# Optimization experiments

Hardware: AMD Instinct MI355X
Metric: run time of the kernel (lower is better)

The kernel has to match this reference:

```python
import jax, jax.numpy as jnp
import numpy as np

B = 64        # graphs in batch
N = 2048      # nodes per graph (uniform -> static pooled sizes)
DEG = 16      # avg degree
E = B * N * DEG
F0 = 128      # node feature dim


def setup_inputs() -> dict:
    key = jax.random.key(0)
    ks = jax.random.split(key, 24)
    x = jax.random.normal(ks[0], (B * N, F0), dtype=jnp.float32)
    # within-graph random edges, PyG batched-graph layout (contiguous node blocks)
    loc = jax.random.randint(ks[1], (2, B, N * DEG), 0, N)
    off = (jnp.arange(B, dtype=jnp.int32) * N)[:, None]
    src = (loc[0].astype(jnp.int32) + off).reshape(-1)
    dst = (loc[1].astype(jnp.int32) + off).reshape(-1)
    g = lambda i, shp: jax.random.normal(ks[i], shp, dtype=jnp.float32) * 0.05
    return {
        'x': x, 'src': src, 'dst': dst,
        'w1l': g(2, (128, 128)), 'b1': jnp.zeros((128,), jnp.float32), 'w1r': g(3, (128, 128)), 'pw1': g(4, (128,)),
        'w2l': g(5, (128, 128)), 'b2': jnp.zeros((128,), jnp.float32), 'w2r': g(6, (128, 128)), 'pw2': g(7, (128,)),
        'w3l': g(8, (128, 128)), 'b3': jnp.zeros((128,), jnp.float32), 'w3r': g(9, (128, 128)), 'pw3': g(10, (128,)),
        'l1w': g(11, (256, 128)), 'l1b': jnp.zeros((128,), jnp.float32),
        'l2w': g(12, (128, 64)), 'l2b': jnp.zeros((64,), jnp.float32),
        'l3w': g(13, (64, 2)), 'l3b': jnp.zeros((2,), jnp.float32),
    }


def _sage(x, src, dst, em, n_nodes, Wl, b, Wr):
    # PyG SAGEConv: lin_l(mean_{j->i} x_j) + lin_r(x_i); edge mask zeroes dropped edges
    msg = x[src] * em[:, None]                                   # [E, F] gather
    agg = jax.ops.segment_sum(msg, dst, num_segments=n_nodes)
    cnt = jax.ops.segment_sum(em, dst, num_segments=n_nodes)
    mean = agg / jnp.maximum(cnt, 1.0)[:, None]
    return mean @ Wl + b + x @ Wr


def _topk_pool(x, src, dst, em, b_graphs, n_per, w):
    # PyG TopKPooling (min_score=None): score = tanh(x@w/||w||), keep top ratio per graph,
    # gate kept features by score, drop edges touching removed nodes, relabel.
    score = jnp.tanh((x @ w) / jnp.linalg.norm(w))
    k = n_per // 2                                               # ratio = 0.5
    _, idx = jax.lax.top_k(score.reshape(b_graphs, n_per), k)    # per-graph local idx
    perm = (jnp.arange(b_graphs, dtype=jnp.int32)[:, None] * n_per + idx.astype(jnp.int32)).reshape(-1)
    xn = x[perm] * score[perm][:, None]
    ntot = b_graphs * n_per
    kept = jnp.zeros((ntot,), bool).at[perm].set(True)
    newidx = jnp.zeros((ntot,), jnp.int32).at[perm].set(jnp.arange(b_graphs * k, dtype=jnp.int32))
    emn = em * kept[src].astype(em.dtype) * kept[dst].astype(em.dtype)
    return xn, newidx[src], newidx[dst], emn, k


def _readout(x, b_graphs, n_per):
    r = x.reshape(b_graphs, n_per, -1)
    return jnp.concatenate([r.max(axis=1), r.mean(axis=1)], axis=1)  # [B, 2F]


def _forward(x, src, dst, w1l, b1, w1r, pw1, w2l, b2, w2r, pw2, w3l, b3, w3r, pw3,
             l1w, l1b, l2w, l2b, l3w, l3b):
    em = jnp.ones((src.shape[0],), x.dtype)
    n = N
    h = jax.nn.relu(_sage(x, src, dst, em, B * n, w1l, b1, w1r))
    h, src, dst, em, n = _topk_pool(h, src, dst, em, B, n, pw1)
    x1 = _readout(h, B, n)
    h = jax.nn.relu(_sage(h, src, dst, em, B * n, w2l, b2, w2r))
    h, src, dst, em, n = _topk_pool(h, src, dst, em, B, n, pw2)
    x2 = _readout(h, B, n)
    h = jax.nn.relu(_sage(h, src, dst, em, B * n, w3l, b3, w3r))
    h, src, dst, em, n = _topk_pool(h, src, dst, em, B, n, pw3)
    x3 = _readout(h, B, n)
    z = x1 + x2 + x3
    z = jax.nn.relu(z @ l1w + l1b)            # dropout is identity in eval mode
    z = jax.nn.relu(z @ l2w + l2b)
    z = z @ l3w + l3b
    return jax.nn.log_softmax(z, axis=-1)


def reference(x, src, dst, w1l, b1, w1r, pw1, w2l, b2, w2r, pw2, w3l, b3, w3r, pw3,
              l1w, l1b, l2w, l2b, l3w, l3b):
    return _forward(x, src, dst, w1l, b1, w1r, pw1, w2l, b2, w2r, pw2, w3l, b3, w3r, pw3,
                    l1w, l1b, l2w, l2b, l3w, l3b)
```

## Files before the change

kernel.cpp:

```cpp
#include <hip/hip_runtime.h>
#include <cmath>

#define NT1  131072
#define ETOT 2097152
#define NB   64
#define F    128
#define CPAD 32
#define RCH  16

__global__ void hist_kernel(const int* __restrict__ dst, int* __restrict__ deg) {
  int e = blockIdx.x * blockDim.x + threadIdx.x;
  if (e < ETOT) atomicAdd(&deg[dst[e]], 1);
}

__global__ void scan1_kernel(const int* __restrict__ deg, int* __restrict__ rowstart,
                             int* __restrict__ bsum) {
  __shared__ int ls[256];
  int base = blockIdx.x * 1024;
  int t = threadIdx.x;
  int i = base + t * 4;
  int a0 = deg[i], a1 = deg[i + 1], a2 = deg[i + 2], a3 = deg[i + 3];
  int s = a0 + a1 + a2 + a3;
  ls[t] = s;
  __syncthreads();
  for (int off = 1; off < 256; off <<= 1) {
    int v = (t >= off) ? ls[t - off] : 0;
    __syncthreads();
    ls[t] += v;
    __syncthreads();
  }
  int excl = ls[t] - s;
  rowstart[i]     = excl;
  rowstart[i + 1] = excl + a0;
  rowstart[i + 2] = excl + a0 + a1;
  rowstart[i + 3] = excl + a0 + a1 + a2;
  if (t == 255) bsum[blockIdx.x] = ls[255];
}

__global__ void scan2_kernel(int* __restrict__ bsum) {
  __shared__ int ls[128];
  int t = threadIdx.x;
  int v0 = bsum[t];
  ls[t] = v0;
  __syncthreads();
  for (int off = 1; off < 128; off <<= 1) {
    int v = (t >= off) ? ls[t - off] : 0;
    __syncthreads();
    ls[t] += v;
    __syncthreads();
  }
  bsum[t] = ls[t] - v0;
}

__global__ void scan3_kernel(int* __restrict__ rowstart, const int* __restrict__ bsum) {
  int base = blockIdx.x * 1024;
  int off = bsum[blockIdx.x];
  int i = base + threadIdx.x * 4;
  rowstart[i] += off; rowstart[i + 1] += off; rowstart[i + 2] += off; rowstart[i + 3] += off;
}

__global__ void fill_kernel(const int* __restrict__ src, const int* __restrict__ dst,
                            const int* __restrict__ rowstart, int* __restrict__ cursor,
                            int* __restrict__ csr) {
  int e = blockIdx.x * blockDim.x + threadIdx.x;
  if (e < ETOT) {
    int d = dst[e];
    int pos = rowstart[d] + atomicAdd(&cursor[d], 1);
    csr[pos] = src[e];
  }
}

__global__ void init_id_kernel(int* __restrict__ m, int* __restrict__ orig,
                               const int* __restrict__ rowstart,
                               const int* __restrict__ deg, int2* __restrict__ sd2) {
  int v = blockIdx.x * blockDim.x + threadIdx.x;
  m[v] = v; orig[v] = v;
  sd2[v] = make_int2(rowstart[v], deg[v]);
}

__global__ void map_kernel(const int* __restrict__ csr, const int* __restrict__ m,
                           int* __restrict__ mcsr) {
  int e = blockIdx.x * blockDim.x + threadIdx.x;
  int4 v = ((const int4*)csr)[e];
  int4 o;
  o.x = m[v.x]; o.y = m[v.y]; o.z = m[v.z]; o.w = m[v.w];
  ((int4*)mcsr)[e] = o;
}

__global__ __launch_bounds__(256) void agg_kernel(
    const float* __restrict__ xin, const int* __restrict__ mcsr,
    const int2* __restrict__ sd2, float* __restrict__ agg,
    const float* __restrict__ pw, float* __restrict__ invn) {
  if (blockIdx.x == 0 && threadIdx.x < 64) {
    int l = threadIdx.x;
    float vv = pw[l] * pw[l] + pw[l + 64] * pw[l + 64];
    #pragma unroll
    for (int o = 32; o; o >>= 1) vv += __shfl_xor(vv, o);
    if (l == 0) *invn = 1.0f / sqrtf(vv);
  }
  int swz = gridDim.x >> 3;
  int nb  = (blockIdx.x & 7) * swz + (blockIdx.x >> 3);
  int g = threadIdx.x >> 5, l = threadIdx.x & 31;
  int jd = nb * 8 + g;
  int2 sdv = sd2[jd];
  int s = sdv.x, d = sdv.y;
  float4 acc = make_float4(0.f, 0.f, 0.f, 0.f);
  int c = 0;
  for (int base = 0; base < d; base += 32) {
    int dc = min(32, d - base);
    int nbid = (l < dc) ? mcsr[s + base + l] : -1;
    int j = 0;
    for (; j + 4 <= dc; j += 4) {
      int n0 = __shfl(nbid, j, 32);
      int n1 = __shfl(nbid, j + 1, 32);
      int n2 = __shfl(nbid, j + 2, 32);
      int n3 = __shfl(nbid, j + 3, 32);
      float4 v0 = *(const float4*)(xin + (size_t)max(n0, 0) * F + l * 4);
      float4 v1 = *(const float4*)(xin + (size_t)max(n1, 0) * F + l * 4);
      float4 v2 = *(const float4*)(xin + (size_t)max(n2, 0) * F + l * 4);
      float4 v3 = *(const float4*)(xin + (size_t)max(n3, 0) * F + l * 4);
      if (n0 >= 0) { acc.x += v0.x; acc.y += v0.y; acc.z += v0.z; acc.w += v0.w; ++c; }
      if (n1 >= 0) { acc.x += v1.x; acc.y += v1.y; acc.z += v1.z; acc.w += v1.w; ++c; }
      if (n2 >= 0) { acc.x += v2.x; acc.y += v2.y; acc.z += v2.z; acc.w += v2.w; ++c; }
      if (n3 >= 0) { acc.x += v3.x; acc.y += v3.y; acc.z += v3.z; acc.w += v3.w; ++c; }
    }
    for (; j < dc; ++j) {
      int n0 = __shfl(nbid, j, 32);
      if (n0 >= 0) {
        float4 v0 = *(const float4*)(xin + (size_t)n0 * F + l * 4);
        acc.x += v0.x; acc.y += v0.y; acc.z += v0.z; acc.w += v0.w; ++c;
      }
    }
  }
  float inv = 1.0f / (float)max(c, 1);
  acc.x *= inv; acc.y *= inv; acc.z *= inv; acc.w *= inv;
  *(float4*)(agg + (size_t)jd * F + l * 4) = acc;
}

__global__ __launch_bounds__(256) void sage_gemm(
    const float* agg, const float* __restrict__ x,
    const float* __restrict__ Wl, const float* __restrict__ Wr,
    const float* __restrict__ bias, float* h,
    const float* __restrict__ pw, const float* __restrict__ invn,
    float* __restrict__ score) {
  __shared__ float At[16][132];
  __shared__ float Wt[16][132];
  int t  = threadIdx.x;
  int tx = t & 15, ty = t >> 4;
  int i0 = blockIdx.x * 128;
  int arow = t & 127, akc = (t >> 7) * 8;
  int wkr  = t >> 4,  wc0 = (t & 15) * 8;

  float acc[8][8];
  #pragma unroll
  for (int r = 0; r < 8; ++r)
    #pragma unroll
    for (int c = 0; c < 8; ++c) acc[r][c] = 0.f;

  for (int kt = 0; kt < 256; kt += 16) {
    const float* Asrc = (kt < 128) ? agg : x;
    int acol = (kt & 127) + akc;
    float4 va0 = *(const float4*)(Asrc + (size_t)(i0 + arow) * F + acol);
    float4 va1 = *(const float4*)(Asrc + (size_t)(i0 + arow) * F + acol + 4);
    const float* Wsrc = ((kt < 128) ? Wl : Wr) + (size_t)((kt & 127) + wkr) * F + wc0;
    float4 vw0 = *(const float4*)(Wsrc);
    float4 vw1 = *(const float4*)(Wsrc + 4);
    __syncthreads();
    At[akc + 0][arow] = va0.x; At[akc + 1][arow] = va0.y;
    At[akc + 2][arow] = va0.z; At[akc + 3][arow] = va0.w;
    At[akc + 4][arow] = va1.x; At[akc + 5][arow] = va1.y;
    At[akc + 6][arow] = va1.z; At[akc + 7][arow] = va1.w;
    Wt[wkr][wc0 + 0] = vw0.x; Wt[wkr][wc0 + 1] = vw0.y;
    Wt[wkr][wc0 + 2] = vw0.z; Wt[wkr][wc0 + 3] = vw0.w;
    Wt[wkr][wc0 + 4] = vw1.x; Wt[wkr][wc0 + 5] = vw1.y;
    Wt[wkr][wc0 + 6] = vw1.z; Wt[wkr][wc0 + 7] = vw1.w;
    __syncthreads();
    #pragma unroll
    for (int k = 0; k < 16; ++k) {
      float4 a0 = *(float4*)(&At[k][ty * 4]);
      float4 a1 = *(float4*)(&At[k][64 + ty * 4]);
      float4 w0 = *(float4*)(&Wt[k][tx * 4]);
      float4 w1 = *(float4*)(&Wt[k][64 + tx * 4]);
      float ar[8] = {a0.x, a0.y, a0.z, a0.w, a1.x, a1.y, a1.z, a1.w};
      float wr[8] = {w0.x, w0.y, w0.z, w0.w, w1.x, w1.y, w1.z, w1.w};
      #pragma unroll
      for (int r = 0; r < 8; ++r)
        #pragma unroll
        for (int c = 0; c < 8; ++c)
          acc[r][c] += ar[r] * wr[c];
    }
  }

  float4 bb0 = *(const float4*)(bias + tx * 4);
  float4 bb1 = *(const float4*)(bias + 64 + tx * 4);
  float4 pw0 = *(const float4*)(pw + tx * 4);
  float4 pw1 = *(const float4*)(pw + 64 + tx * 4);
  float inorm = *invn;
  #pragma unroll
  for (int r = 0; r < 8; ++r) {
    int row = i0 + ((r < 4) ? (ty * 4 + r) : (64 + ty * 4 + r - 4));
    float4 o0, o1;
    o0.x = fmaxf(acc[r][0] + bb0.x, 0.f);
    o0.y = fmaxf(acc[r][1] + bb0.y, 0.f);
    o0.z = fmaxf(acc[r][2] + bb0.z, 0.f);
    o0.w = fmaxf(acc[r][3] + bb0.w, 0.f);
    o1.x = fmaxf(acc[r][4] + bb1.x, 0.f);
    o1.y = fmaxf(acc[r][5] + bb1.y, 0.f);
    o1.z = fmaxf(acc[r][6] + bb1.z, 0.f);
    o1.w = fmaxf(acc[r][7] + bb1.w, 0.f);
    *(float4*)(h + (size_t)row * F + tx * 4) = o0;
    *(float4*)(h + (size_t)row * F + 64 + tx * 4) = o1;
    float p = o0.x * pw0.x + o0.y * pw0.y + o0.z * pw0.z + o0.w * pw0.w
            + o1.x * pw1.x + o1.y * pw1.y + o1.z * pw1.z + o1.w * pw1.w;
    #pragma unroll
    for (int off = 8; off; off >>= 1) p += __shfl_xor(p, off);
    if (tx == 0) score[row] = tanhf(p * inorm);
  }
}

__global__ void topk_kernel(const float* __restrict__ score, float* __restrict__ thr,
                            int* __restrict__ quota, int* __restrict__ tiecur,
                            int* __restrict__ curg, int nper, int k) {
  __shared__ float s[2048];
  __shared__ int cnts[256];
  int b = blockIdx.x, tid = threadIdx.x;
  for (int i = tid; i < nper; i += 256) s[i] = score[b * nper + i];
  __syncthreads();
  for (int size = 2; size <= nper; size <<= 1)
    for (int stride = size >> 1; stride; stride >>= 1) {
      for (int i = tid; i < nper; i += 256) {
        int j = i ^ stride;
        if (j > i) {
          bool up = ((i & size) == 0);
          float a = s[i], c = s[j];
          if ((a > c) == up) { s[i] = c; s[j] = a; }
        }
      }
      __syncthreads();
    }
  float T = s[nper - k];
  int c = 0;
  for (int i = tid; i < nper; i += 256) c += (s[i] > T) ? 1 : 0;
  cnts[tid] = c;
  __syncthreads();
  for (int st = 128; st; st >>= 1) {
    if (tid < st) cnts[tid] += cnts[tid + st];
    __syncthreads();
  }
  if (tid == 0) { thr[b] = T; quota[b] = k - cnts[0]; tiecur[b * CPAD] = 0; curg[b * CPAD] = 0; }
}

__global__ __launch_bounds__(256) void select_kernel(
    const float* __restrict__ h, const float* __restrict__ score,
    const float* __restrict__ thr, const int* __restrict__ quota,
    int* __restrict__ tiecur, int* __restrict__ curg,
    const int* __restrict__ origA, int* __restrict__ origB,
    int* __restrict__ m, float* __restrict__ xnext,
    const int* __restrict__ rowstart, const int* __restrict__ deg,
    int2* __restrict__ sd2, int nper, int k) {
  __shared__ int   snid[64];
  __shared__ float ssc[64];
  int t = threadIdx.x;
  int base = blockIdx.x * 64;
  int b = base / nper;
  if (t < 64) {
    int i = base + t;
    float sc = score[i];
    float T = thr[b];
    int keep = (sc > T) ? 1 : 0;
    if (!keep && sc == T) keep = (atomicAdd(&tiecur[b * CPAD], 1) < quota[b]) ? 1 : 0;
    unsigned long long mask = __ballot(keep);
    int pre = __popcll(mask & ((1ull << t) - 1ull));
    int tot = __popcll(mask);
    int wbase = 0;
    if (t == 0 && tot) wbase = atomicAdd(&curg[b * CPAD], tot);
    wbase = __shfl(wbase, 0);
    int nid = keep ? (b * k + wbase + pre) : -1;
    int orig = origA[i];
    m[orig] = nid;
    if (nid >= 0) {
      origB[nid] = orig;
      sd2[nid] = make_int2(rowstart[orig], deg[orig]);
    }
    snid[t] = nid; ssc[t] = sc;
  }
  __syncthreads();
  int g = t >> 5, l32 = t & 31;
  for (int n = g; n < 64; n += 8) {
    int nid = snid[n];
    if (nid >= 0) {
      float sc = ssc[n];
      float4 v = *(const float4*)(h + (size_t)(base + n) * F + l32 * 4);
      v.x *= sc; v.y *= sc; v.z *= sc; v.w *= sc;
      *(float4*)(xnext + (size_t)nid * F + l32 * 4) = v;
    }
  }
}

__global__ __launch_bounds__(256) void readout_partial(
    const float* __restrict__ xp, float* __restrict__ pmax,
    float* __restrict__ psum, int k) {
  __shared__ float smax[256], ssum[256];
  int b  = blockIdx.x >> 4;
  int ch = blockIdx.x & 15;
  int t  = threadIdx.x;
  int rg = t >> 7, f = t & 127;
  int rows = k >> 4;
  int r0 = ch * rows;
  const float* base = xp + ((size_t)b * k + r0) * F;
  float mx = -INFINITY, sm = 0.f;
  #pragma unroll 4
  for (int r = rg; r < rows; r += 2) {
    float v = base[(size_t)r * F + f];
    mx = fmaxf(mx, v);
    sm += v;
  }
  smax[t] = mx; ssum[t] = sm;
  __syncthreads();
  if (t < 128) {
    int o = (b * 16 + ch) * 128 + t;
    pmax[o] = fmaxf(smax[t], smax[t + 128]);
    psum[o] = ssum[t] + ssum[t + 128];
  }
}

__global__ void readout_final(const float* __restrict__ pmax,
                              const float* __restrict__ psum,
                              float* __restrict__ z, int k) {
  int b = blockIdx.x, f = threadIdx.x;
  float mx = -INFINITY, sm = 0.f;
  #pragma unroll
  for (int ch = 0; ch < 16; ++ch) {
    int o = (b * 16 + ch) * 128 + f;
    mx = fmaxf(mx, pmax[o]);
    sm += psum[o];
  }
  z[b * 256 + f]       += mx;
  z[b * 256 + 128 + f] += sm / (float)k;
}

__global__ void mlp_kernel(const float* __restrict__ z,
                           const float* __restrict__ l1w, const float* __restrict__ l1b,
                           const float* __restrict__ l2w, const float* __restrict__ l2b,
                           const float* __restrict__ l3w, const float* __restrict__ l3b,
                           float* __restrict__ out) {
  int b = blockIdx.x, t = threadIdx.x;
  __shared__ float zz[256], o1[128], o2[64], lg[2];
  zz[t]       = z[b * 256 + t];
  zz[t + 128] = z[b * 256 + 128 + t];
  __syncthreads();
  float a = l1b[t];
  for (int i = 0; i < 256; ++i) a += zz[i] * l1w[i * 128 + t];
  o1[t] = fmaxf(a, 0.f);
  __syncthreads();
  if (t < 64) {
    float a2 = l2b[t];
    for (int i = 0; i < 128; ++i) a2 += o1[i] * l2w[i * 64 + t];
    o2[t] = fmaxf(a2, 0.f);
  }
  __syncthreads();
  if (t < 2) {
    float a3 = l3b[t];
    for (int i = 0; i < 64; ++i) a3 += o2[i] * l3w[i * 2 + t];
    lg[t] = a3;
  }
  __syncthreads();
  if (t == 0) {
    float mmax = fmaxf(lg[0], lg[1]);
    float lse = mmax + logf(expf(lg[0] - mmax) + expf(lg[1] - mmax));
    out[b * 2 + 0] = lg[0] - lse;
    out[b * 2 + 1] = lg[1] - lse;
  }
}

extern "C" void kernel_launch(void* const* d_in, const int* in_sizes, int n_in,
                              void* d_out, int out_size, void* d_ws, size_t ws_size,
                              hipStream_t stream) {
  const float* x   = (const float*)d_in[0];
  const int*   src = (const int*)d_in[1];
  const int*   dst = (const int*)d_in[2];
  const float* Wl[3] = {(const float*)d_in[3], (const float*)d_in[7],  (const float*)d_in[11]};
  const float* bs[3] = {(const float*)d_in[4], (const float*)d_in[8],  (const float*)d_in[12]};
  const float* Wr[3] = {(const float*)d_in[5], (const float*)d_in[9],  (const float*)d_in[13]};
  const float* pw[3] = {(const float*)d_in[6], (const float*)d_in[10], (const float*)d_in[14]};
  const float* l1w = (const float*)d_in[15]; const float* l1b = (const float*)d_in[16];
  const float* l2w = (const float*)d_in[17]; const float* l2b = (const float*)d_in[18];
  const float* l3w = (const float*)d_in[19]; const float* l3b = (const float*)d_in[20];
  float* out = (float*)d_out;

  char* p = (char*)d_ws;
  auto take = [&](size_t bytes) { char* q = p; p += (bytes + 255) & ~(size_t)255; return q; };
  float* aggh   = (float*)take((size_t)NT1 * F * 4);
  float* xbuf   = (float*)take((size_t)65536 * F * 4);
  float* score  = (float*)take((size_t)NT1 * 4);
  int* deg      = (int*)take((size_t)NT1 * 4);
  int* rowstart = (int*)take((size_t)NT1 * 4);
  int* cursor   = (int*)take((size_t)NT1 * 4);
  int* m        = (int*)take((size_t)NT1 * 4);
  int* origA    = (int*)take((size_t)NT1 * 4);
  int* origB    = (int*)take((size_t)NT1 * 4);
  int2* sd2     = (int2*)take((size_t)NT1 * 8);
  int* csr      = (int*)take((size_t)ETOT * 4);
  int* mcsr     = (int*)take((size_t)ETOT * 4);
  int* bsum     = (int*)take(128 * 4);
  float* thr    = (float*)take(NB * 4);
  int* quota    = (int*)take(NB * 4);
  int* tiecur   = (int*)take(NB * CPAD * 4);
  int* curg     = (int*)take(NB * CPAD * 4);
  float* z      = (float*)take(NB * 256 * 4);
  float* pmax   = (float*)take((size_t)NB * RCH * F * 4);
  float* psum   = (float*)take((size_t)NB * RCH * F * 4);
  float* invn   = (float*)take(4);

  hipMemsetAsync(deg, 0, (size_t)NT1 * 4, stream);
  hipMemsetAsync(cursor, 0, (size_t)NT1 * 4, stream);
  hipMemsetAsync(z, 0, (size_t)NB * 256 * 4, stream);

  hist_kernel<<<ETOT / 256, 256, 0, stream>>>(dst, deg);
  scan1_kernel<<<128, 256, 0, stream>>>(deg, rowstart, bsum);
  scan2_kernel<<<1, 128, 0, stream>>>(bsum);
  scan3_kernel<<<128, 256, 0, stream>>>(rowstart, bsum);
  fill_kernel<<<ETOT / 256, 256, 0, stream>>>(src, dst, rowstart, cursor, csr);
  init_id_kernel<<<NT1 / 256, 256, 0, stream>>>(m, origA, rowstart, deg, sd2);

  int NT = NT1, nper = 2048;
  const float* xin = x;
  int* oin = origA; int* oout = origB;
  for (int s = 0; s < 3; ++s) {
    int k = nper / 2;
    const int* edges = csr;
    if (s > 0) {
      map_kernel<<<ETOT / 4 / 256, 256, 0, stream>>>(csr, m, mcsr);
      edges = mcsr;
    }
    agg_kernel<<<NT / 8, 256, 0, stream>>>(xin, edges, sd2, aggh, pw[s], invn);
    sage_gemm<<<NT / 128, 256, 0, stream>>>(aggh, xin, Wl[s], Wr[s], bs[s], aggh,
                                            pw[s], invn, score);
    topk_kernel<<<NB, 256, 0, stream>>>(score, thr, quota, tiecur, curg, nper, k);
    select_kernel<<<NT / 64, 256, 0, stream>>>(aggh, score, thr, quota, tiecur, curg,
                                               oin, oout, m, xbuf, rowstart, deg, sd2,
                                               nper, k);
    readout_partial<<<NB * RCH, 256, 0, stream>>>(xbuf, pmax, psum, k);
    readout_final<<<NB, 128, 0, stream>>>(pmax, psum, z, k);
    NT = NB * k; nper = k; xin = xbuf;
    int* tmp = oin; oin = oout; oout = tmp;
  }
  mlp_kernel<<<NB, 128, 0, stream>>>(z, l1w, l1b, l2w, l2b, l3w, l3b, out);
}
```

Measured before the change: 763.1 us.

## Use radix-select top-k, double-buffer SAGE GEMM, fuse readout into select

The per-graph bitonic sort in topk is replaced with an 8-bit radix select over order-preserving uint keys, which finds the k-th score threshold and tie quota with far fewer shared-memory passes. sage_gemm is templated on row-tile size, uses double-buffered shared tiles with register prefetch of the next K tile, and uses 64-row tiles for the smaller pooled stages so more blocks are launched. The readout partial max and sum are folded into select_kernel, which removes the readout_partial launch and a re-read of the pooled features. The cost is a more complex GEMM with extra shared memory and per-block partials sized by MAXBLK.

```diff
diff --git a/kernel.cpp b/kernel.cpp
--- a/kernel.cpp
+++ b/kernel.cpp
@@ -6,7 +6,7 @@
 #define NB   64
 #define F    128
 #define CPAD 32
-#define RCH  16
+#define MAXBLK 32
 
 __global__ void hist_kernel(const int* __restrict__ dst, int* __restrict__ deg) {
   int e = blockIdx.x * blockDim.x + threadIdx.x;
@@ -137,57 +137,76 @@
   *(float4*)(agg + (size_t)jd * F + l * 4) = acc;
 }
 
+template <int BM>
 __global__ __launch_bounds__(256) void sage_gemm(
     const float* agg, const float* __restrict__ x,
     const float* __restrict__ Wl, const float* __restrict__ Wr,
     const float* __restrict__ bias, float* h,
     const float* __restrict__ pw, const float* __restrict__ invn,
     float* __restrict__ score) {
-  __shared__ float At[16][132];
-  __shared__ float Wt[16][132];
+  constexpr int RQ = BM / 64;
+  __shared__ float At[2][16][BM + 4];
+  __shared__ float Wt[2][16][132];
   int t  = threadIdx.x;
   int tx = t & 15, ty = t >> 4;
-  int i0 = blockIdx.x * 128;
-  int arow = t & 127, akc = (t >> 7) * 8;
-  int wkr  = t >> 4,  wc0 = (t & 15) * 8;
-
-  float acc[8][8];
+  int i0 = blockIdx.x * BM;
+  int arow, akc;
+  if (BM == 128) { arow = t & 127; akc = (t >> 7) * 8; }
+  else           { arow = t & 63;  akc = (t >> 6) * 4; }
+  int wkr = t >> 4, wc0 = (t & 15) * 8;
+
+  float4 va0, va1, vw0, vw1;
+  auto loadT = [&](int ktile) {
+    const float* Asrc = (ktile < 8) ? agg : x;
+    int acol = (ktile & 7) * 16 + akc;
+    const float* pA = Asrc + (size_t)(i0 + arow) * F + acol;
+    va0 = *(const float4*)pA;
+    if (BM == 128) va1 = *(const float4*)(pA + 4);
+    const float* Wsrc = ((ktile < 8) ? Wl : Wr) + (size_t)((ktile & 7) * 16 + wkr) * F + wc0;
+    vw0 = *(const float4*)Wsrc;
+    vw1 = *(const float4*)(Wsrc + 4);
+  };
+
+  float acc[4 * RQ][8];
   #pragma unroll
-  for (int r = 0; r < 8; ++r)
+  for (int r = 0; r < 4 * RQ; ++r)
     #pragma unroll
     for (int c = 0; c < 8; ++c) acc[r][c] = 0.f;
 
-  for (int kt = 0; kt < 256; kt += 16) {
-    const float* Asrc = (kt < 128) ? agg : x;
-    int acol = (kt & 127) + akc;
-    float4 va0 = *(const float4*)(Asrc + (size_t)(i0 + arow) * F + acol);
-    float4 va1 = *(const float4*)(Asrc + (size_t)(i0 + arow) * F + acol + 4);
-    const float* Wsrc = ((kt < 128) ? Wl : Wr) + (size_t)((kt & 127) + wkr) * F + wc0;
-    float4 vw0 = *(const float4*)(Wsrc);
-    float4 vw1 = *(const float4*)(Wsrc + 4);
-    __syncthreads();
-    At[akc + 0][arow] = va0.x; At[akc + 1][arow] = va0.y;
-    At[akc + 2][arow] = va0.z; At[akc + 3][arow] = va0.w;
-    At[akc + 4][arow] = va1.x; At[akc + 5][arow] = va1.y;
-    At[akc + 6][arow] = va1.z; At[akc + 7][arow] = va1.w;
-    Wt[wkr][wc0 + 0] = vw0.x; Wt[wkr][wc0 + 1] = vw0.y;
-    Wt[wkr][wc0 + 2] = vw0.z; Wt[wkr][wc0 + 3] = vw0.w;
-    Wt[wkr][wc0 + 4] = vw1.x; Wt[wkr][wc0 + 5] = vw1.y;
-    Wt[wkr][wc0 + 6] = vw1.z; Wt[wkr][wc0 + 7] = vw1.w;
-    __syncthreads();
+  loadT(0);
+  for (int kt = 0; kt < 16; ++kt) {
+    int buf = kt & 1;
+    At[buf][akc + 0][arow] = va0.x; At[buf][akc + 1][arow] = va0.y;
+    At[buf][akc + 2][arow] = va0.z; At[buf][akc + 3][arow] = va0.w;
+    if (BM == 128) {
+      At[buf][akc + 4][arow] = va1.x; At[buf][akc + 5][arow] = va1.y;
+      At[buf][akc + 6][arow] = va1.z; At[buf][akc + 7][arow] = va1.w;
+    }
+    *(float4*)(&Wt[buf][wkr][wc0]) = vw0;
+    *(float4*)(&Wt[buf][wkr][wc0 + 4]) = vw1;
+    __syncthreads();
+    if (kt < 15) loadT(kt + 1);
     #pragma unroll
     for (int k = 0; k < 16; ++k) {
-      float4 a0 = *(float4*)(&At[k][ty * 4]);
-      float4 a1 = *(float4*)(&At[k][64 + ty * 4]);
-      float4 w0 = *(float4*)(&Wt[k][tx * 4]);
-      float4 w1 = *(float4*)(&Wt[k][64 + tx * 4]);
-      float ar[8] = {a0.x, a0.y, a0.z, a0.w, a1.x, a1.y, a1.z, a1.w};
+      float4 a0 = *(float4*)(&At[buf][k][ty * 4]);
+      float4 w0 = *(float4*)(&Wt[buf][k][tx * 4]);
+      float4 w1 = *(float4*)(&Wt[buf][k][64 + tx * 4]);
       float wr[8] = {w0.x, w0.y, w0.z, w0.w, w1.x, w1.y, w1.z, w1.w};
+      float ar0[4] = {a0.x, a0.y, a0.z, a0.w};
       #pragma unroll
-      for (int r = 0; r < 8; ++r)
+      for (int r = 0; r < 4; ++r)
         #pragma unroll
         for (int c = 0; c < 8; ++c)
-          acc[r][c] += ar[r] * wr[c];
+          acc[r][c] += ar0[r] * wr[c];
+      if (RQ == 2) {
+        float4 a1 = *(float4*)(&At[buf][k][64 + ty * 4]);
+        float ar1[4] = {a1.x, a1.y, a1.z, a1.w};
+        #pragma unroll
+        for (int r = 0; r < 4; ++r)
+          #pragma unroll
+          for (int c = 0; c < 8; ++c)
+            acc[4 + r][c] += ar1[r] * wr[c];
+      }
     }
   }
 
@@ -197,7 +216,7 @@
   float4 pw1 = *(const float4*)(pw + 64 + tx * 4);
   float inorm = *invn;
   #pragma unroll
-  for (int r = 0; r < 8; ++r) {
+  for (int r = 0; r < 4 * RQ; ++r) {
     int row = i0 + ((r < 4) ? (ty * 4 + r) : (64 + ty * 4 + r - 4));
     float4 o0, o1;
     o0.x = fmaxf(acc[r][0] + bb0.x, 0.f);
@@ -218,36 +237,51 @@
   }
 }
 
-__global__ void topk_kernel(const float* __restrict__ score, float* __restrict__ thr,
-                            int* __restrict__ quota, int* __restrict__ tiecur,
-                            int* __restrict__ curg, int nper, int k) {
-  __shared__ float s[2048];
-  __shared__ int cnts[256];
-  int b = blockIdx.x, tid = threadIdx.x;
-  for (int i = tid; i < nper; i += 256) s[i] = score[b * nper + i];
-  __syncthreads();
-  for (int size = 2; size <= nper; size <<= 1)
-    for (int stride = size >> 1; stride; stride >>= 1) {
-      for (int i = tid; i < nper; i += 256) {
-        int j = i ^ stride;
-        if (j > i) {
-          bool up = ((i & size) == 0);
-          float a = s[i], c = s[j];
-          if ((a > c) == up) { s[i] = c; s[j] = a; }
-        }
-      }
+__global__ __launch_bounds__(256) void topk_kernel(
+    const float* __restrict__ score, float* __restrict__ thr,
+    int* __restrict__ quota, int* __restrict__ tiecur,
+    int* __restrict__ curg, int nper, int k) {
+  __shared__ unsigned su[2048];
+  __shared__ int hist[256];
+  __shared__ int vsel;
+  int b = blockIdx.x, t = threadIdx.x;
+  for (int i = t; i < nper; i += 256) {
+    unsigned u = __float_as_uint(score[b * nper + i]);
+    su[i] = (u & 0x80000000u) ? ~u : (u | 0x80000000u);
+  }
+  __syncthreads();
+  unsigned prefix = 0;
+  int rem = k;
+  for (int shift = 24; shift >= 0; shift -= 8) {
+    hist[t] = 0;
+    __syncthreads();
+    unsigned maskhi = (shift == 24) ? 0u : (0xFFFFFFFFu << (shift + 8));
+    for (int i = t; i < nper; i += 256) {
+      unsigned u = su[i];
+      if ((u & maskhi) == prefix) atomicAdd(&hist[(u >> shift) & 255], 1);
+    }
+    __syncthreads();
+    for (int off = 1; off < 256; off <<= 1) {
+      int v = (t + off < 256) ? hist[t + off] : 0;
       __syncthreads();
-    }
-  float T = s[nper - k];
-  int c = 0;
-  for (int i = tid; i < nper; i += 256) c += (s[i] > T) ? 1 : 0;
-  cnts[tid] = c;
-  __syncthreads();
-  for (int st = 128; st; st >>= 1) {
-    if (tid < st) cnts[tid] += cnts[tid + st];
-    __syncthreads();
-  }
-  if (tid == 0) { thr[b] = T; quota[b] = k - cnts[0]; tiecur[b * CPAD] = 0; curg[b * CPAD] = 0; }
+      hist[t] += v;
+      __syncthreads();
+    }
+    if (hist[t] >= rem && (t == 255 || hist[t + 1] < rem)) vsel = t;
+    __syncthreads();
+    int v = vsel;
+    int above = (v == 255) ? 0 : hist[v + 1];
+    rem -= above;
+    prefix |= ((unsigned)v << shift);
+    __syncthreads();
+  }
+  if (t == 0) {
+    unsigned s = prefix;
+    unsigned ub = (s >> 31) ? (s & 0x7FFFFFFFu) : ~s;
+    thr[b] = __uint_as_float(ub);
+    quota[b] = rem;
+    tiecur[b * CPAD] = 0; curg[b * CPAD] = 0;
+  }
 }
 
 __global__ __launch_bounds__(256) void select_kernel(
@@ -257,9 +291,11 @@
     const int* __restrict__ origA, int* __restrict__ origB,
     int* __restrict__ m, float* __restrict__ xnext,
     const int* __restrict__ rowstart, const int* __restrict__ deg,
-    int2* __restrict__ sd2, int nper, int k) {
+    int2* __restrict__ sd2, float* __restrict__ pmax, float* __restrict__ psum,
+    int nper, int k) {
   __shared__ int   snid[64];
   __shared__ float ssc[64];
+  __shared__ float smax[8][128], ssum[8][128];
   int t = threadIdx.x;
   int base = blockIdx.x * 64;
   int b = base / nper;
@@ -286,6 +322,8 @@
   }
   __syncthreads();
   int g = t >> 5, l32 = t & 31;
+  float4 pm = make_float4(-INFINITY, -INFINITY, -INFINITY, -INFINITY);
+  float4 ps = make_float4(0.f, 0.f, 0.f, 0.f);
   for (int n = g; n < 64; n += 8) {
     int nid = snid[n];
     if (nid >= 0) {
@@ -293,45 +331,35 @@
       float4 v = *(const float4*)(h + (size_t)(base + n) * F + l32 * 4);
       v.x *= sc; v.y *= sc; v.z *= sc; v.w *= sc;
       *(float4*)(xnext + (size_t)nid * F + l32 * 4) = v;
-    }
-  }
-}
-
-__global__ __launch_bounds__(256) void readout_partial(
-    const float* __restrict__ xp, float* __restrict__ pmax,
-    float* __restrict__ psum, int k) {
-  __shared__ float smax[256], ssum[256];
-  int b  = blockIdx.x >> 4;
-  int ch = blockIdx.x & 15;
-  int t  = threadIdx.x;
-  int rg = t >> 7, f = t & 127;
-  int rows = k >> 4;
-  int r0 = ch * rows;
-  const float* base = xp + ((size_t)b * k + r0) * F;
-  float mx = -INFINITY, sm = 0.f;
-  #pragma unroll 4
-  for (int r = rg; r < rows; r += 2) {
-    float v = base[(size_t)r * F + f];
-    mx = fmaxf(mx, v);
-    sm += v;
-  }
-  smax[t] = mx; ssum[t] = sm;
+      pm.x = fmaxf(pm.x, v.x); pm.y = fmaxf(pm.y, v.y);
+      pm.z = fmaxf(pm.z, v.z); pm.w = fmaxf(pm.w, v.w);
+      ps.x += v.x; ps.y += v.y; ps.z += v.z; ps.w += v.w;
+    }
+  }
+  *(float4*)(&smax[g][l32 * 4]) = pm;
+  *(float4*)(&ssum[g][l32 * 4]) = ps;
   __syncthreads();
   if (t < 128) {
-    int o = (b * 16 + ch) * 128 + t;
-    pmax[o] = fmaxf(smax[t], smax[t + 128]);
-    psum[o] = ssum[t] + ssum[t + 128];
+    float mx = -INFINITY, sm = 0.f;
+    #pragma unroll
+    for (int gg = 0; gg < 8; ++gg) {
+      mx = fmaxf(mx, smax[gg][t]);
+      sm += ssum[gg][t];
+    }
+    int nblk = nper >> 6;
+    int blkpos = blockIdx.x - b * nblk;
+    int o = (b * MAXBLK + blkpos) * 128 + t;
+    pmax[o] = mx; psum[o] = sm;
   }
 }
 
 __global__ void readout_final(const float* __restrict__ pmax,
                               const float* __restrict__ psum,
-                              float* __restrict__ z, int k) {
+                              float* __restrict__ z, int k, int nblk) {
   int b = blockIdx.x, f = threadIdx.x;
   float mx = -INFINITY, sm = 0.f;
-  #pragma unroll
-  for (int ch = 0; ch < 16; ++ch) {
-    int o = (b * 16 + ch) * 128 + f;
+  for (int ch = 0; ch < nblk; ++ch) {
+    int o = (b * MAXBLK + ch) * 128 + f;
     mx = fmaxf(mx, pmax[o]);
     sm += psum[o];
   }
@@ -408,8 +436,8 @@
   int* tiecur   = (int*)take(NB * CPAD * 4);
   int* curg     = (int*)take(NB * CPAD * 4);
   float* z      = (float*)take(NB * 256 * 4);
-  float* pmax   = (float*)take((size_t)NB * RCH * F * 4);
-  float* psum   = (float*)take((size_t)NB * RCH * F * 4);
+  float* pmax   = (float*)take((size_t)NB * MAXBLK * F * 4);
+  float* psum   = (float*)take((size_t)NB * MAXBLK * F * 4);
   float* invn   = (float*)take(4);
 
   hipMemsetAsync(deg, 0, (size_t)NT1 * 4, stream);
@@ -434,14 +462,17 @@
       edges = mcsr;
     }
     agg_kernel<<<NT / 8, 256, 0, stream>>>(xin, edges, sd2, aggh, pw[s], invn);
-    sage_gemm<<<NT / 128, 256, 0, stream>>>(aggh, xin, Wl[s], Wr[s], bs[s], aggh,
-                                            pw[s], invn, score);
+    if (s == 0)
+      sage_gemm<128><<<NT / 128, 256, 0, stream>>>(aggh, xin, Wl[s], Wr[s], bs[s], aggh,
+                                                   pw[s], invn, score);
+    else
+      sage_gemm<64><<<NT / 64, 256, 0, stream>>>(aggh, xin, Wl[s], Wr[s], bs[s], aggh,
+                                                 pw[s], invn, score);
     topk_kernel<<<NB, 256, 0, stream>>>(score, thr, quota, tiecur, curg, nper, k);
     select_kernel<<<NT / 64, 256, 0, stream>>>(aggh, score, thr, quota, tiecur, curg,
                                                oin, oout, m, xbuf, rowstart, deg, sd2,
-                                               nper, k);
-    readout_partial<<<NB * RCH, 256, 0, stream>>>(xbuf, pmax, psum, k);
-    readout_final<<<NB, 128, 0, stream>>>(pmax, psum, z, k);
+                                               pmax, psum, nper, k);
+    readout_final<<<NB, 128, 0, stream>>>(pmax, psum, z, k, nper >> 6);
     NT = NB * k; nper = k; xin = xbuf;
     int* tmp = oin; oin = oout; oout = tmp;
   }
```

New measurement: 701.9 us. -8.0%, faster.
